# Kernel tuning notes

Hardware: AMD Instinct MI355X
Metric: run time of the kernel (lower is better)

## Reference

```python
import jax, jax.numpy as jnp
import numpy as np

GRAVITY = 9.81
W_INERTIA = 1.0
W_GRAVITY = 0.01
W_STRAIN = 1.0

V = 500_000
E = 2_000_000


def setup_inputs() -> dict:
    key = jax.random.key(0)
    ks = jax.random.split(key, 7)
    pos_next = jax.random.normal(ks[0], (V, 3), dtype=jnp.float32)
    pos_curr = jax.random.normal(ks[1], (V, 3), dtype=jnp.float32)
    pos_prev = jax.random.normal(ks[2], (V, 3), dtype=jnp.float32)
    mass = jax.random.uniform(ks[3], (V, 1), dtype=jnp.float32)
    elements = jax.random.randint(ks[4], (E, 4), 0, V, dtype=jnp.int64)
    rest_volumes = jax.random.uniform(ks[5], (E,), dtype=jnp.float32)
    rest_inv = jax.random.normal(ks[6], (E, 3, 3), dtype=jnp.float32)
    lam = jnp.float32(1.0)
    mu = jnpp_one = jnp.float32(1.0)
    return {
        "pos_next": pos_next, "pos_curr": pos_curr, "pos_prev": pos_prev,
        "mass": mass, "elements": elements, "rest_volumes": rest_volumes,
        "rest_inv": rest_inv, "lam": lam, "mu": mu,
    }


def _det3(F):
    # F: (E, 3, 3)
    return (F[:, 0, 0] * (F[:, 1, 1] * F[:, 2, 2] - F[:, 1, 2] * F[:, 2, 1])
            - F[:, 0, 1] * (F[:, 1, 0] * F[:, 2, 2] - F[:, 1, 2] * F[:, 2, 0])
            + F[:, 0, 2] * (F[:, 1, 0] * F[:, 2, 1] - F[:, 1, 1] * F[:, 2, 0]))


def _physics_loss(pos_next, pos_curr, pos_prev, mass, elements, rest_volumes, rest_inv, lam, mu):
    # Inertia: mean over all V*3 entries of 0.5 * m * a^2
    accel = pos_next + pos_prev - 2.0 * pos_curr          # (V, 3)
    inertia = 0.5 * jnp.mean(mass * accel * accel)
    # Gravity: -mean(m * g * y)
    gravity = -jnp.mean(mass * GRAVITY * pos_curr[:, 1:2])
    # Strain (Neo-Hookean) on pos_next
    v = pos_next[elements]                                 # (E, 4, 3)
    Ds = jnp.stack([v[:, 1] - v[:, 0], v[:, 2] - v[:, 0], v[:, 3] - v[:, 0]], axis=-1)  # (E,3,3)
    F_def = jnp.einsum('eij,ejk->eik', Ds, rest_inv)       # (E, 3, 3)
    det_F = jnp.maximum(_det3(F_def), 1e-8)
    log_det = jnp.log(det_F)
    tr_FtF = jnp.sum(F_def * F_def, axis=(1, 2))           # trace(F^T F) = ||F||_F^2
    psi = 0.5 * lam * log_det ** 2 - mu * log_det + 0.5 * mu * (tr_FtF - 3.0)
    strain = jnp.mean(psi * rest_volumes)
    return W_INERTIA * inertia + W_GRAVITY * gravity + W_STRAIN * strain


def reference(pos_next, pos_curr, pos_prev, mass, elements, rest_volumes, rest_inv, lam, mu):
    return _physics_loss(pos_next, pos_curr, pos_prev, mass, elements, rest_volumes, rest_inv, lam, mu)
```

## Files before the change

kernel.cpp:

```cpp
#include <hip/hip_runtime.h>

#define GRAVITY_F 9.81f
#define EPT 2

typedef int   v4i __attribute__((ext_vector_type(4)));
typedef float v4f __attribute__((ext_vector_type(4), aligned(4)));

__device__ __forceinline__ float blockReduceSum(float val) {
    #pragma unroll
    for (int off = 32; off > 0; off >>= 1)
        val += __shfl_down(val, off, 64);
    __shared__ float smem[16];
    const int lane = threadIdx.x & 63;
    const int wave = threadIdx.x >> 6;
    if (lane == 0) smem[wave] = val;
    __syncthreads();
    const int nwaves = (blockDim.x + 63) >> 6;
    val = 0.0f;
    if (wave == 0) {
        if (lane < nwaves) val = smem[lane];
        #pragma unroll
        for (int off = 8; off > 0; off >>= 1)
            val += __shfl_down(val, off, 64);
    }
    return val;
}

__global__ void __launch_bounds__(256, 4)
fused_kernel(const float* __restrict__ pn,
             const float* __restrict__ pc,
             const float* __restrict__ pp,
             const float* __restrict__ mass,
             const int*   __restrict__ elems,
             const float* __restrict__ vols,
             const float* __restrict__ rinv,
             const float* __restrict__ lam_p,
             const float* __restrict__ mu_p,
             float* __restrict__ partials,
             int V, int E, int Eblocks,
             float sI, float sG, float sS) {
    float local = 0.0f;

    if ((int)blockIdx.x < Eblocks) {
        const float lam = lam_p[0];
        const float mu  = mu_p[0];
        const int base = blockIdx.x * (EPT * 256) + threadIdx.x;

        int   ec[EPT];
        float sc[EPT];
        #pragma unroll
        for (int i = 0; i < EPT; ++i) {
            const int e = base + i * 256;
            ec[i] = e < E ? e : (E - 1);
            sc[i] = e < E ? sS : 0.0f;
        }

        v4i idx[EPT];
        #pragma unroll
        for (int i = 0; i < EPT; ++i)
            idx[i] = __builtin_nontemporal_load(((const v4i*)elems) + ec[i]);

        v4f rA[EPT], rB[EPT];
        float rC[EPT], vol[EPT];
        #pragma unroll
        for (int i = 0; i < EPT; ++i) {
            const float* Rp = rinv + 9 * (size_t)ec[i];
            rA[i]  = __builtin_nontemporal_load((const v4f*)Rp);
            rB[i]  = __builtin_nontemporal_load((const v4f*)(Rp + 4));
            rC[i]  = __builtin_nontemporal_load(Rp + 8);
            vol[i] = __builtin_nontemporal_load(vols + ec[i]);
        }

        const int cap = 3 * V - 4;
        v4f q[EPT][4];
        #pragma unroll
        for (int i = 0; i < EPT; ++i) {
            #pragma unroll
            for (int j = 0; j < 4; ++j) {
                int off = 3 * idx[i][j];
                off = off > cap ? cap : off;
                q[i][j] = *reinterpret_cast<const v4f*>(pn + off);
            }
        }

        asm volatile("" ::
            "v"(q[0][0]), "v"(q[0][1]), "v"(q[0][2]), "v"(q[0][3]),
            "v"(q[1][0]), "v"(q[1][1]), "v"(q[1][2]), "v"(q[1][3]),
            "v"(rA[0]), "v"(rB[0]), "v"(rA[1]), "v"(rB[1]),
            "v"(rC[0]), "v"(rC[1]), "v"(vol[0]), "v"(vol[1]));

        const int lastV = V - 1;
        #pragma unroll
        for (int i = 0; i < EPT; ++i) {
            float x[4][3];
            #pragma unroll
            for (int j = 0; j < 4; ++j) {
                const bool sh = (idx[i][j] == lastV);
                x[j][0] = sh ? q[i][j][1] : q[i][j][0];
                x[j][1] = sh ? q[i][j][2] : q[i][j][1];
                x[j][2] = sh ? q[i][j][3] : q[i][j][2];
            }
            const float R[9] = { rA[i][0], rA[i][1], rA[i][2], rA[i][3],
                                 rB[i][0], rB[i][1], rB[i][2], rB[i][3],
                                 rC[i] };
            float d[3][3];
            #pragma unroll
            for (int r = 0; r < 3; ++r) {
                d[r][0] = x[1][r] - x[0][r];
                d[r][1] = x[2][r] - x[0][r];
                d[r][2] = x[3][r] - x[0][r];
            }
            float F[3][3];
            #pragma unroll
            for (int r = 0; r < 3; ++r)
                #pragma unroll
                for (int k = 0; k < 3; ++k)
                    F[r][k] = d[r][0] * R[0 * 3 + k]
                            + d[r][1] * R[1 * 3 + k]
                            + d[r][2] * R[2 * 3 + k];
            const float det = F[0][0] * (F[1][1] * F[2][2] - F[1][2] * F[2][1])
                            - F[0][1] * (F[1][0] * F[2][2] - F[1][2] * F[2][0])
                            + F[0][2] * (F[1][0] * F[2][1] - F[1][1] * F[2][0]);
            const float ld = logf(fmaxf(det, 1e-8f));
            float tr = 0.0f;
            #pragma unroll
            for (int r = 0; r < 3; ++r)
                #pragma unroll
                for (int k = 0; k < 3; ++k)
                    tr += F[r][k] * F[r][k];
            const float psi = 0.5f * lam * ld * ld - mu * ld + 0.5f * mu * (tr - 3.0f);
            local += sc[i] * (psi * vol[i]);
        }
    } else {
        const int v = (blockIdx.x - Eblocks) * blockDim.x + threadIdx.x;
        if (v < V) {
            const float m  = __builtin_nontemporal_load(mass + v);
            const float p0 = __builtin_nontemporal_load(pc + 3 * v + 0);
            const float y  = __builtin_nontemporal_load(pc + 3 * v + 1);
            const float p2 = __builtin_nontemporal_load(pc + 3 * v + 2);
            const float n0 = __builtin_nontemporal_load(pn + 3 * v + 0);
            const float n1 = __builtin_nontemporal_load(pn + 3 * v + 1);
            const float n2 = __builtin_nontemporal_load(pn + 3 * v + 2);
            const float q0 = __builtin_nontemporal_load(pp + 3 * v + 0);
            const float q1 = __builtin_nontemporal_load(pp + 3 * v + 1);
            const float q2 = __builtin_nontemporal_load(pp + 3 * v + 2);
            const float a0 = n0 + q0 - 2.0f * p0;
            const float a1 = n1 + q1 - 2.0f * y;
            const float a2 = n2 + q2 - 2.0f * p2;
            local = sI * (m * (a0 * a0 + a1 * a1 + a2 * a2)) + sG * (m * y);
        }
    }

    const float tot = blockReduceSum(local);
    if (threadIdx.x == 0) partials[blockIdx.x] = tot;
}

__global__ void reduce_kernel(const float* __restrict__ partials, int n,
                              float* __restrict__ out) {
    double s = 0.0;
    for (int i = threadIdx.x; i < n; i += blockDim.x)
        s += (double)partials[i];
    __shared__ double sm[256];
    sm[threadIdx.x] = s;
    __syncthreads();
    #pragma unroll
    for (int off = 128; off > 0; off >>= 1) {
        if (threadIdx.x < off) sm[threadIdx.x] += sm[threadIdx.x + off];
        __syncthreads();
    }
    if (threadIdx.x == 0) out[0] = (float)sm[0];
}

extern "C" void kernel_launch(void* const* d_in, const int* in_sizes, int n_in,
                              void* d_out, int out_size, void* d_ws, size_t ws_size,
                              hipStream_t stream) {
    const float* pos_next = (const float*)d_in[0];
    const float* pos_curr = (const float*)d_in[1];
    const float* pos_prev = (const float*)d_in[2];
    const float* mass     = (const float*)d_in[3];
    const int*   elements = (const int*)d_in[4];
    const float* rest_vol = (const float*)d_in[5];
    const float* rest_inv = (const float*)d_in[6];
    const float* lam_p    = (const float*)d_in[7];
    const float* mu_p     = (const float*)d_in[8];
    float* out = (float*)d_out;

    const int V = in_sizes[3];
    const int E = in_sizes[5];

    const float sI = 0.5f / (3.0f * (float)V);
    const float sG = -0.01f * GRAVITY_F / (float)V;
    const float sS = 1.0f / (float)E;

    const int block = 256;
    const int Eblocks = (E + EPT * block - 1) / (EPT * block);
    const int Vblocks = (V + block - 1) / block;
    const int grid = Eblocks + Vblocks;

    float* partials = (float*)d_ws;

    fused_kernel<<<grid, block, 0, stream>>>(pos_next, pos_curr, pos_prev,
                                             mass, elements, rest_vol,
                                             rest_inv, lam_p, mu_p,
                                             partials, V, E, Eblocks,
                                             sI, sG, sS);
    reduce_kernel<<<1, 256, 0, stream>>>(partials, grid, out);
}
```

Baseline: 218.6 us.

## Vectorize vertex pass, run it first, and use scalar gathers for elements

The per-vertex inertia/gravity pass now handles four vertices per thread with 16-byte vector loads. These blocks are placed at the front of the grid so they run first, and pos_next is loaded with normal loads so it stays warm in cache for the element gathers. The element path drops the unaligned 16-byte gather with clamp-and-shift fixup in favour of three scalar loads per vertex. This trades the shift logic for more load instructions. The intent is fewer memory transactions in the vertex stage and better cache reuse of pos_next.

```diff
diff --git a/kernel.cpp b/kernel.cpp
--- a/kernel.cpp
+++ b/kernel.cpp
@@ -3,8 +3,9 @@
 #define GRAVITY_F 9.81f
 #define EPT 2
 
-typedef int   v4i __attribute__((ext_vector_type(4)));
-typedef float v4f __attribute__((ext_vector_type(4), aligned(4)));
+typedef int   v4i  __attribute__((ext_vector_type(4)));
+typedef float v4f  __attribute__((ext_vector_type(4), aligned(16)));
+typedef float v4fu __attribute__((ext_vector_type(4), aligned(4)));
 
 __device__ __forceinline__ float blockReduceSum(float val) {
     #pragma unroll
@@ -37,14 +38,15 @@
              const float* __restrict__ lam_p,
              const float* __restrict__ mu_p,
              float* __restrict__ partials,
-             int V, int E, int Eblocks,
+             int V, int E, int Vblocks4,
              float sI, float sG, float sS) {
     float local = 0.0f;
 
-    if ((int)blockIdx.x < Eblocks) {
+    if ((int)blockIdx.x >= Vblocks4) {
         const float lam = lam_p[0];
         const float mu  = mu_p[0];
-        const int base = blockIdx.x * (EPT * 256) + threadIdx.x;
+        const int eb   = blockIdx.x - Vblocks4;
+        const int base = eb * (EPT * 256) + threadIdx.x;
 
         int   ec[EPT];
         float sc[EPT];
@@ -60,55 +62,56 @@
         for (int i = 0; i < EPT; ++i)
             idx[i] = __builtin_nontemporal_load(((const v4i*)elems) + ec[i]);
 
-        v4f rA[EPT], rB[EPT];
+        v4fu rA[EPT], rB[EPT];
         float rC[EPT], vol[EPT];
         #pragma unroll
         for (int i = 0; i < EPT; ++i) {
             const float* Rp = rinv + 9 * (size_t)ec[i];
-            rA[i]  = __builtin_nontemporal_load((const v4f*)Rp);
-            rB[i]  = __builtin_nontemporal_load((const v4f*)(Rp + 4));
+            rA[i]  = __builtin_nontemporal_load((const v4fu*)Rp);
+            rB[i]  = __builtin_nontemporal_load((const v4fu*)(Rp + 4));
             rC[i]  = __builtin_nontemporal_load(Rp + 8);
             vol[i] = __builtin_nontemporal_load(vols + ec[i]);
         }
 
-        const int cap = 3 * V - 4;
-        v4f q[EPT][4];
-        #pragma unroll
-        for (int i = 0; i < EPT; ++i) {
-            #pragma unroll
-            for (int j = 0; j < 4; ++j) {
-                int off = 3 * idx[i][j];
-                off = off > cap ? cap : off;
-                q[i][j] = *reinterpret_cast<const v4f*>(pn + off);
+        float x[EPT][4][3];
+        #pragma unroll
+        for (int i = 0; i < EPT; ++i) {
+            const float* v0 = pn + 3 * (size_t)idx[i].x;
+            const float* v1 = pn + 3 * (size_t)idx[i].y;
+            const float* v2 = pn + 3 * (size_t)idx[i].z;
+            const float* v3 = pn + 3 * (size_t)idx[i].w;
+            #pragma unroll
+            for (int r = 0; r < 3; ++r) {
+                x[i][0][r] = v0[r];
+                x[i][1][r] = v1[r];
+                x[i][2][r] = v2[r];
+                x[i][3][r] = v3[r];
             }
         }
 
         asm volatile("" ::
-            "v"(q[0][0]), "v"(q[0][1]), "v"(q[0][2]), "v"(q[0][3]),
-            "v"(q[1][0]), "v"(q[1][1]), "v"(q[1][2]), "v"(q[1][3]),
+            "v"(x[0][0][0]), "v"(x[0][0][1]), "v"(x[0][0][2]),
+            "v"(x[0][1][0]), "v"(x[0][1][1]), "v"(x[0][1][2]),
+            "v"(x[0][2][0]), "v"(x[0][2][1]), "v"(x[0][2][2]),
+            "v"(x[0][3][0]), "v"(x[0][3][1]), "v"(x[0][3][2]),
+            "v"(x[1][0][0]), "v"(x[1][0][1]), "v"(x[1][0][2]),
+            "v"(x[1][1][0]), "v"(x[1][1][1]), "v"(x[1][1][2]),
+            "v"(x[1][2][0]), "v"(x[1][2][1]), "v"(x[1][2][2]),
+            "v"(x[1][3][0]), "v"(x[1][3][1]), "v"(x[1][3][2]),
             "v"(rA[0]), "v"(rB[0]), "v"(rA[1]), "v"(rB[1]),
             "v"(rC[0]), "v"(rC[1]), "v"(vol[0]), "v"(vol[1]));
 
-        const int lastV = V - 1;
-        #pragma unroll
-        for (int i = 0; i < EPT; ++i) {
-            float x[4][3];
-            #pragma unroll
-            for (int j = 0; j < 4; ++j) {
-                const bool sh = (idx[i][j] == lastV);
-                x[j][0] = sh ? q[i][j][1] : q[i][j][0];
-                x[j][1] = sh ? q[i][j][2] : q[i][j][1];
-                x[j][2] = sh ? q[i][j][3] : q[i][j][2];
-            }
+        #pragma unroll
+        for (int i = 0; i < EPT; ++i) {
             const float R[9] = { rA[i][0], rA[i][1], rA[i][2], rA[i][3],
                                  rB[i][0], rB[i][1], rB[i][2], rB[i][3],
                                  rC[i] };
             float d[3][3];
             #pragma unroll
             for (int r = 0; r < 3; ++r) {
-                d[r][0] = x[1][r] - x[0][r];
-                d[r][1] = x[2][r] - x[0][r];
-                d[r][2] = x[3][r] - x[0][r];
+                d[r][0] = x[i][1][r] - x[i][0][r];
+                d[r][1] = x[i][2][r] - x[i][0][r];
+                d[r][2] = x[i][3][r] - x[i][0][r];
             }
             float F[3][3];
             #pragma unroll
@@ -132,22 +135,47 @@
             local += sc[i] * (psi * vol[i]);
         }
     } else {
-        const int v = (blockIdx.x - Eblocks) * blockDim.x + threadIdx.x;
-        if (v < V) {
-            const float m  = __builtin_nontemporal_load(mass + v);
-            const float p0 = __builtin_nontemporal_load(pc + 3 * v + 0);
-            const float y  = __builtin_nontemporal_load(pc + 3 * v + 1);
-            const float p2 = __builtin_nontemporal_load(pc + 3 * v + 2);
-            const float n0 = __builtin_nontemporal_load(pn + 3 * v + 0);
-            const float n1 = __builtin_nontemporal_load(pn + 3 * v + 1);
-            const float n2 = __builtin_nontemporal_load(pn + 3 * v + 2);
-            const float q0 = __builtin_nontemporal_load(pp + 3 * v + 0);
-            const float q1 = __builtin_nontemporal_load(pp + 3 * v + 1);
-            const float q2 = __builtin_nontemporal_load(pp + 3 * v + 2);
-            const float a0 = n0 + q0 - 2.0f * p0;
-            const float a1 = n1 + q1 - 2.0f * y;
-            const float a2 = n2 + q2 - 2.0f * p2;
-            local = sI * (m * (a0 * a0 + a1 * a1 + a2 * a2)) + sG * (m * y);
+        const int g  = blockIdx.x * blockDim.x + threadIdx.x;
+        const int v0 = g * 4;
+        if (v0 + 4 <= V) {
+            const v4f m4 = *(const v4f*)(mass + v0);
+            const v4f n0 = *(const v4f*)(pn + 3 * v0);
+            const v4f n1 = *(const v4f*)(pn + 3 * v0 + 4);
+            const v4f n2 = *(const v4f*)(pn + 3 * v0 + 8);
+            const v4f c0 = __builtin_nontemporal_load((const v4f*)(pc + 3 * v0));
+            const v4f c1 = __builtin_nontemporal_load((const v4f*)(pc + 3 * v0 + 4));
+            const v4f c2 = __builtin_nontemporal_load((const v4f*)(pc + 3 * v0 + 8));
+            const v4f q0 = __builtin_nontemporal_load((const v4f*)(pp + 3 * v0));
+            const v4f q1 = __builtin_nontemporal_load((const v4f*)(pp + 3 * v0 + 4));
+            const v4f q2 = __builtin_nontemporal_load((const v4f*)(pp + 3 * v0 + 8));
+            const v4f N[3] = { n0, n1, n2 };
+            const v4f C[3] = { c0, c1, c2 };
+            const v4f Q[3] = { q0, q1, q2 };
+            #pragma unroll
+            for (int i = 0; i < 4; ++i) {
+                float acc = 0.0f;
+                #pragma unroll
+                for (int r = 0; r < 3; ++r) {
+                    const int k = 3 * i + r;
+                    const float a = N[k >> 2][k & 3] + Q[k >> 2][k & 3]
+                                  - 2.0f * C[k >> 2][k & 3];
+                    acc += a * a;
+                }
+                const int ky = 3 * i + 1;
+                const float y = C[ky >> 2][ky & 3];
+                local += sI * (m4[i] * acc) + sG * (m4[i] * y);
+            }
+        } else {
+            for (int v = v0; v < V; ++v) {
+                const float m  = mass[v];
+                const float p0 = pc[3 * v + 0];
+                const float y  = pc[3 * v + 1];
+                const float p2 = pc[3 * v + 2];
+                const float a0 = pn[3 * v + 0] + pp[3 * v + 0] - 2.0f * p0;
+                const float a1 = pn[3 * v + 1] + pp[3 * v + 1] - 2.0f * y;
+                const float a2 = pn[3 * v + 2] + pp[3 * v + 2] - 2.0f * p2;
+                local += sI * (m * (a0 * a0 + a1 * a1 + a2 * a2)) + sG * (m * y);
+            }
         }
     }
 
@@ -193,16 +221,17 @@
     const float sS = 1.0f / (float)E;
 
     const int block = 256;
-    const int Eblocks = (E + EPT * block - 1) / (EPT * block);
-    const int Vblocks = (V + block - 1) / block;
-    const int grid = Eblocks + Vblocks;
+    const int Eblocks  = (E + EPT * block - 1) / (EPT * block);
+    const int Vgroups  = (V + 3) / 4;
+    const int Vblocks4 = (Vgroups + block - 1) / block;
+    const int grid = Vblocks4 + Eblocks;
 
     float* partials = (float*)d_ws;
 
     fused_kernel<<<grid, block, 0, stream>>>(pos_next, pos_curr, pos_prev,
                                              mass, elements, rest_vol,
                                              rest_inv, lam_p, mu_p,
-                                             partials, V, E, Eblocks,
+                                             partials, V, E, Vblocks4,
                                              sI, sG, sS);
     reduce_kernel<<<1, 256, 0, stream>>>(partials, grid, out);
 }
```

After: 217.9 us. Within noise of the previous version (-0.3%).
